# Kernel optimization log

Hardware: AMD Instinct MI355X
Metric: run time of the kernel (lower is better)

## Reference

```python
import jax, jax.numpy as jnp
import numpy as np

RADIUS = 0.5
NEG_INF = -jnp.inf


def setup_inputs() -> dict:
    key = jax.random.key(0)
    ks = jax.random.split(key, 10)
    N_q, N_o, pos_dim, latent_dim = 2048, 2048, 3, 64
    enc_dim = 3 * pos_dim  # q_pos, o_pos, rel
    inp = {
        "h_obs": jax.random.normal(ks[0], (N_o, latent_dim), dtype=jnp.float32),
        "x_obs": jax.random.normal(ks[1], (N_o, latent_dim), dtype=jnp.float32),
        "pos_obs": jax.random.uniform(ks[2], (N_o, pos_dim), dtype=jnp.float32),
        "pos_query": jax.random.uniform(ks[3], (N_q, pos_dim), dtype=jnp.float32),
        # kernel_mlp: Linear(enc_dim->latent) + ReLU + Linear(latent->1)
        "W1": jax.random.normal(ks[4], (enc_dim, latent_dim), dtype=jnp.float32) / np.sqrt(enc_dim),
        "b1": jnp.zeros((latent_dim,), dtype=jnp.float32),
        "W2": jax.random.normal(ks[5], (latent_dim, 1), dtype=jnp.float32) / np.sqrt(latent_dim),
        "b2": jnp.zeros((1,), dtype=jnp.float32),
        # value_proj: Linear(latent->latent)
        "Wv": jax.random.normal(ks[6], (latent_dim, latent_dim), dtype=jnp.float32) / np.sqrt(latent_dim),
        "bv": jnp.zeros((latent_dim,), dtype=jnp.float32),
    }
    return inp


def reference(h_obs, x_obs, pos_obs, pos_query, W1, b1, W2, b2, Wv, bv):
    # rel: [N_q, N_o, pos_dim]
    rel = pos_query[:, None, :] - pos_obs[None, :, :]
    N_q, N_o, _ = rel.shape
    pos_q_exp = jnp.broadcast_to(pos_query[:, None, :], rel.shape)
    pos_o_exp = jnp.broadcast_to(pos_obs[None, :, :], rel.shape)
    kernel_input = jnp.concatenate([pos_q_exp, pos_o_exp, rel], axis=-1)  # [N_q, N_o, 3*pos_dim]
    # small pointwise MLP over all pairs
    hidden = jax.nn.relu(jnp.einsum('qoe,el->qol', kernel_input, W1) + b1)  # [N_q, N_o, latent]
    logits = jnp.einsum('qol,lk->qok', hidden, W2)[..., 0] + b2[0]          # [N_q, N_o]
    # radius mask
    dist = jnp.linalg.norm(rel, axis=-1)
    logits = jnp.where(dist > RADIUS, NEG_INF, logits)
    # softmax over observations (dim=1)
    weights = jax.nn.softmax(logits, axis=1)  # [N_q, N_o]
    v = h_obs @ Wv + bv                        # [N_o, latent]
    h_query = weights @ v                      # [N_q, latent]
    return h_query
```

## Files before the change

kernel.cpp:

```cpp
#include <hip/hip_runtime.h>

#define NQ 2048
#define NO 2048
#define NOC 32

constexpr size_t OFF_T  = 0;
constexpr size_t OFF_PH = (size_t)NO * 64;
constexpr size_t OFF_PS = OFF_PH + (size_t)NOC * NQ * 64;

__global__ __launch_bounds__(256) void gano_prep(
    const float* __restrict__ pos_obs,
    const float* __restrict__ W1,
    float* __restrict__ T)
{
    int gid = blockIdx.x * 256 + threadIdx.x;
    int o = gid >> 6, l = gid & 63;
    float po0 = pos_obs[o * 3 + 0], po1 = pos_obs[o * 3 + 1], po2 = pos_obs[o * 3 + 2];
    float w3 = W1[3 * 64 + l], w4 = W1[4 * 64 + l], w5 = W1[5 * 64 + l];
    float w6 = W1[6 * 64 + l], w7 = W1[7 * 64 + l], w8 = W1[8 * 64 + l];
    T[(size_t)o * 64 + l] = po0 * (w3 - w6) + po1 * (w4 - w7) + po2 * (w5 - w8);
}

__global__ __launch_bounds__(256, 4) void gano_main(
    const float* __restrict__ T,
    const float* __restrict__ h_obs,
    const float* __restrict__ pos_obs,
    const float* __restrict__ pos_query,
    const float* __restrict__ W1,
    const float* __restrict__ b1,
    const float* __restrict__ W2,
    float* __restrict__ Ph,
    float* __restrict__ Ps)
{
    __shared__ float ue[64 * 64];
    __shared__ float sbuf[4 * 64];

    const int tid  = threadIdx.x;
    const int lane = tid & 63;
    const int wave = __builtin_amdgcn_readfirstlane(tid >> 6);
    const int qg = blockIdx.x >> 5;
    const int oc = blockIdx.x & 31;
    const int obase = oc * 64;
    const int q  = qg * 64 + lane;
    const int ow = wave * 16;

    float pq0 = pos_query[q * 3 + 0];
    float pq1 = pos_query[q * 3 + 1];
    float pq2 = pos_query[q * 3 + 2];

    float u[64];
#pragma unroll
    for (int l = 0; l < 64; ++l) {
        float a = b1[l];
        a += pq0 * W1[0 * 64 + l];
        a += pq1 * W1[1 * 64 + l];
        a += pq2 * W1[2 * 64 + l];
        a += pq0 * W1[6 * 64 + l];
        a += pq1 * W1[7 * 64 + l];
        a += pq2 * W1[8 * 64 + l];
        u[l] = a;
    }

    float spart = 0.f;
#pragma unroll 2
    for (int o = 0; o < 16; ++o) {
        const int toff = __builtin_amdgcn_readfirstlane((obase + ow + o) * 64);
        const float* __restrict__ trow = T + toff;
        float a0 = 0.f, a1 = 0.f, a2 = 0.f, a3 = 0.f;
#pragma unroll
        for (int l = 0; l < 64; l += 4) {
            a0 += W2[l + 0] * fmaxf(u[l + 0] + trow[l + 0], 0.f);
            a1 += W2[l + 1] * fmaxf(u[l + 1] + trow[l + 1], 0.f);
            a2 += W2[l + 2] * fmaxf(u[l + 2] + trow[l + 2], 0.f);
            a3 += W2[l + 3] * fmaxf(u[l + 3] + trow[l + 3], 0.f);
        }
        float lgo = (a0 + a1) + (a2 + a3);
        const int poff = __builtin_amdgcn_readfirstlane((obase + ow + o) * 3);
        float d0 = pq0 - pos_obs[poff + 0];
        float d1 = pq1 - pos_obs[poff + 1];
        float d2 = pq2 - pos_obs[poff + 2];
        float dd = d0 * d0 + d1 * d1 + d2 * d2;
        float ev = (dd > 0.25f) ? 0.f : __expf(lgo);
        spart += ev;
        ue[(ow + o) * 64 + lane] = ev;
    }
    sbuf[wave * 64 + lane] = spart;
    __syncthreads();

    float h0 = 0.f, h1 = 0.f, h2 = 0.f, h3 = 0.f, h4 = 0.f, h5 = 0.f, h6 = 0.f, h7 = 0.f;
    float h8 = 0.f, h9 = 0.f, hA = 0.f, hB = 0.f, hC = 0.f, hD = 0.f, hE = 0.f, hF = 0.f;
#pragma unroll 2
    for (int o = 0; o < 64; ++o) {
        float eo = ue[o * 64 + lane];
        const int hoff = __builtin_amdgcn_readfirstlane((obase + o) * 64 + ow);
        const float* __restrict__ hr = h_obs + hoff;
        h0 += eo * hr[0];  h1 += eo * hr[1];  h2 += eo * hr[2];  h3 += eo * hr[3];
        h4 += eo * hr[4];  h5 += eo * hr[5];  h6 += eo * hr[6];  h7 += eo * hr[7];
        h8 += eo * hr[8];  h9 += eo * hr[9];  hA += eo * hr[10]; hB += eo * hr[11];
        hC += eo * hr[12]; hD += eo * hr[13]; hE += eo * hr[14]; hF += eo * hr[15];
    }

    float* hp = Ph + ((size_t)oc * NQ + (size_t)qg * 64 + lane) * 64 + ow;
    ((float4*)hp)[0] = make_float4(h0, h1, h2, h3);
    ((float4*)hp)[1] = make_float4(h4, h5, h6, h7);
    ((float4*)hp)[2] = make_float4(h8, h9, hA, hB);
    ((float4*)hp)[3] = make_float4(hC, hD, hE, hF);
    if (wave == 0) {
        float s = sbuf[lane] + sbuf[64 + lane] + sbuf[128 + lane] + sbuf[192 + lane];
        Ps[(size_t)oc * NQ + (size_t)qg * 64 + lane] = s;
    }
}

__global__ __launch_bounds__(256, 2) void gano_comb(
    const float* __restrict__ Ph,
    const float* __restrict__ Ps,
    const float* __restrict__ Wv,
    const float* __restrict__ bv,
    float* __restrict__ out)
{
    __shared__ __align__(16) float wv[64 * 64];
    __shared__ __align__(16) float g[4 * 68];
    const int tid  = threadIdx.x;
    const int lane = tid & 63;
    const int wave = tid >> 6;
    const int q0 = blockIdx.x * 4;
    {
        const float4* src = (const float4*)Wv;
        float4* dst = (float4*)wv;
#pragma unroll
        for (int k = 0; k < 4; ++k) dst[tid + k * 256] = src[tid + k * 256];
    }
    {
        const int qi = wave, k = lane;
        float acc = 0.f;
#pragma unroll
        for (int c = 0; c < NOC; ++c)
            acc += Ph[((size_t)c * NQ + q0 + qi) * 64 + k];
        g[qi * 68 + k] = acc;
        if (k == 0) {
            float ss = 0.f;
#pragma unroll
            for (int c = 0; c < NOC; ++c) ss += Ps[(size_t)c * NQ + q0 + qi];
            g[qi * 68 + 64] = ss;
        }
    }
    __syncthreads();
    const float* gq = g + wave * 68;
    float inv = 1.0f / gq[64];
    float a0 = 0.f, a1 = 0.f, a2 = 0.f, a3 = 0.f;
#pragma unroll
    for (int kb = 0; kb < 16; ++kb) {
        float4 g4 = *(const float4*)(gq + kb * 4);
        a0 += g4.x * wv[(kb * 4 + 0) * 64 + lane];
        a1 += g4.y * wv[(kb * 4 + 1) * 64 + lane];
        a2 += g4.z * wv[(kb * 4 + 2) * 64 + lane];
        a3 += g4.w * wv[(kb * 4 + 3) * 64 + lane];
    }
    out[(size_t)(q0 + wave) * 64 + lane] = ((a0 + a1) + (a2 + a3)) * inv + bv[lane];
}

extern "C" void kernel_launch(void* const* d_in, const int* in_sizes, int n_in,
                              void* d_out, int out_size, void* d_ws, size_t ws_size,
                              hipStream_t stream) {
    const float* h_obs     = (const float*)d_in[0];
    const float* pos_obs   = (const float*)d_in[2];
    const float* pos_query = (const float*)d_in[3];
    const float* W1        = (const float*)d_in[4];
    const float* b1        = (const float*)d_in[5];
    const float* W2        = (const float*)d_in[6];
    const float* Wv        = (const float*)d_in[8];
    const float* bv        = (const float*)d_in[9];
    float* ws  = (float*)d_ws;
    float* out = (float*)d_out;

    gano_prep<<<dim3(NO * 64 / 256), dim3(256), 0, stream>>>(pos_obs, W1, ws + OFF_T);
    gano_main<<<dim3(1024), dim3(256), 0, stream>>>(ws + OFF_T, h_obs, pos_obs, pos_query,
                                                    W1, b1, W2, ws + OFF_PH, ws + OFF_PS);
    gano_comb<<<dim3(NQ / 4), dim3(256), 0, stream>>>(ws + OFF_PH, ws + OFF_PS, Wv, bv, out);
}
```

Before: 120.8 us.

## Transpose T table and stage per-query hidden bias in LDS to cut registers

New measurement: 117.7 us. -2.6%, faster.

```diff
diff --git a/kernel.cpp b/kernel.cpp
--- a/kernel.cpp
+++ b/kernel.cpp
@@ -4,25 +4,26 @@
 #define NO 2048
 #define NOC 32
 
-constexpr size_t OFF_T  = 0;
-constexpr size_t OFF_PH = (size_t)NO * 64;
+constexpr size_t OFF_TT = 0;
+constexpr size_t OFF_PH = (size_t)64 * NO;
 constexpr size_t OFF_PS = OFF_PH + (size_t)NOC * NQ * 64;
 
 __global__ __launch_bounds__(256) void gano_prep(
     const float* __restrict__ pos_obs,
     const float* __restrict__ W1,
-    float* __restrict__ T)
+    float* __restrict__ Tt)
 {
-    int gid = blockIdx.x * 256 + threadIdx.x;
-    int o = gid >> 6, l = gid & 63;
+    int idx = blockIdx.x * 256 + threadIdx.x;
+    int o = idx & (NO - 1);
+    int l = idx >> 11;
     float po0 = pos_obs[o * 3 + 0], po1 = pos_obs[o * 3 + 1], po2 = pos_obs[o * 3 + 2];
     float w3 = W1[3 * 64 + l], w4 = W1[4 * 64 + l], w5 = W1[5 * 64 + l];
     float w6 = W1[6 * 64 + l], w7 = W1[7 * 64 + l], w8 = W1[8 * 64 + l];
-    T[(size_t)o * 64 + l] = po0 * (w3 - w6) + po1 * (w4 - w7) + po2 * (w5 - w8);
+    Tt[(size_t)l * NO + o] = po0 * (w3 - w6) + po1 * (w4 - w7) + po2 * (w5 - w8);
 }
 
 __global__ __launch_bounds__(256, 4) void gano_main(
-    const float* __restrict__ T,
+    const float* __restrict__ Tt,
     const float* __restrict__ h_obs,
     const float* __restrict__ pos_obs,
     const float* __restrict__ pos_query,
@@ -32,6 +33,7 @@
     float* __restrict__ Ph,
     float* __restrict__ Ps)
 {
+    __shared__ __align__(16) float ut[16 * 64 * 4];
     __shared__ float ue[64 * 64];
     __shared__ float sbuf[4 * 64];
 
@@ -48,39 +50,52 @@
     float pq1 = pos_query[q * 3 + 1];
     float pq2 = pos_query[q * 3 + 2];
 
-    float u[64];
 #pragma unroll
-    for (int l = 0; l < 64; ++l) {
-        float a = b1[l];
-        a += pq0 * W1[0 * 64 + l];
-        a += pq1 * W1[1 * 64 + l];
-        a += pq2 * W1[2 * 64 + l];
-        a += pq0 * W1[6 * 64 + l];
-        a += pq1 * W1[7 * 64 + l];
-        a += pq2 * W1[8 * 64 + l];
-        u[l] = a;
+    for (int k = 0; k < 4; ++k) {
+        const int lb = wave * 4 + k;
+        float4 uv;
+        {
+            const int l = lb * 4;
+            uv.x = b1[l+0] + pq0*W1[l+0] + pq1*W1[64+l+0] + pq2*W1[128+l+0]
+                 + pq0*W1[384+l+0] + pq1*W1[448+l+0] + pq2*W1[512+l+0];
+            uv.y = b1[l+1] + pq0*W1[l+1] + pq1*W1[64+l+1] + pq2*W1[128+l+1]
+                 + pq0*W1[384+l+1] + pq1*W1[448+l+1] + pq2*W1[512+l+1];
+            uv.z = b1[l+2] + pq0*W1[l+2] + pq1*W1[64+l+2] + pq2*W1[128+l+2]
+                 + pq0*W1[384+l+2] + pq1*W1[448+l+2] + pq2*W1[512+l+2];
+            uv.w = b1[l+3] + pq0*W1[l+3] + pq1*W1[64+l+3] + pq2*W1[128+l+3]
+                 + pq0*W1[384+l+3] + pq1*W1[448+l+3] + pq2*W1[512+l+3];
+        }
+        *(float4*)(ut + (size_t)(lb * 64 + lane) * 4) = uv;
     }
+    __syncthreads();
 
+    float lg[16];
+#pragma unroll
+    for (int o = 0; o < 16; ++o) lg[o] = 0.f;
+#pragma unroll
+    for (int lb = 0; lb < 16; ++lb) {
+        float4 u4 = *(const float4*)(ut + (size_t)(lb * 64 + lane) * 4);
+#pragma unroll
+        for (int dl = 0; dl < 4; ++dl) {
+            const int l = lb * 4 + dl;
+            const int toff = __builtin_amdgcn_readfirstlane(l * NO + obase + ow);
+            const float* __restrict__ tr = Tt + toff;
+            const float ul = (dl == 0) ? u4.x : (dl == 1) ? u4.y : (dl == 2) ? u4.z : u4.w;
+            const float wl = W2[l];
+#pragma unroll
+            for (int o = 0; o < 16; ++o)
+                lg[o] += wl * fmaxf(ul + tr[o], 0.f);
+        }
+    }
     float spart = 0.f;
-#pragma unroll 2
+#pragma unroll
     for (int o = 0; o < 16; ++o) {
-        const int toff = __builtin_amdgcn_readfirstlane((obase + ow + o) * 64);
-        const float* __restrict__ trow = T + toff;
-        float a0 = 0.f, a1 = 0.f, a2 = 0.f, a3 = 0.f;
-#pragma unroll
-        for (int l = 0; l < 64; l += 4) {
-            a0 += W2[l + 0] * fmaxf(u[l + 0] + trow[l + 0], 0.f);
-            a1 += W2[l + 1] * fmaxf(u[l + 1] + trow[l + 1], 0.f);
-            a2 += W2[l + 2] * fmaxf(u[l + 2] + trow[l + 2], 0.f);
-            a3 += W2[l + 3] * fmaxf(u[l + 3] + trow[l + 3], 0.f);
-        }
-        float lgo = (a0 + a1) + (a2 + a3);
         const int poff = __builtin_amdgcn_readfirstlane((obase + ow + o) * 3);
         float d0 = pq0 - pos_obs[poff + 0];
         float d1 = pq1 - pos_obs[poff + 1];
         float d2 = pq2 - pos_obs[poff + 2];
         float dd = d0 * d0 + d1 * d1 + d2 * d2;
-        float ev = (dd > 0.25f) ? 0.f : __expf(lgo);
+        float ev = (dd > 0.25f) ? 0.f : __expf(lg[o]);
         spart += ev;
         ue[(ow + o) * 64 + lane] = ev;
     }
@@ -173,8 +188,8 @@
     float* ws  = (float*)d_ws;
     float* out = (float*)d_out;
 
-    gano_prep<<<dim3(NO * 64 / 256), dim3(256), 0, stream>>>(pos_obs, W1, ws + OFF_T);
-    gano_main<<<dim3(1024), dim3(256), 0, stream>>>(ws + OFF_T, h_obs, pos_obs, pos_query,
+    gano_prep<<<dim3(NO * 64 / 256), dim3(256), 0, stream>>>(pos_obs, W1, ws + OFF_TT);
+    gano_main<<<dim3(1024), dim3(256), 0, stream>>>(ws + OFF_TT, h_obs, pos_obs, pos_query,
                                                     W1, b1, W2, ws + OFF_PH, ws + OFF_PS);
     gano_comb<<<dim3(NQ / 4), dim3(256), 0, stream>>>(ws + OFF_PH, ws + OFF_PS, Wv, bv, out);
 }
```

## Fuse obs-projection prep into main kernel with LDS tables and smaller obs chunks

Applied to the files above, without the earlier changes.

After: 122.3 us. No clear change (+1.2%).

```diff
diff --git a/kernel.cpp b/kernel.cpp
--- a/kernel.cpp
+++ b/kernel.cpp
@@ -2,27 +2,12 @@
 
 #define NQ 2048
 #define NO 2048
-#define NOC 32
+#define NOC 64
 
-constexpr size_t OFF_T  = 0;
-constexpr size_t OFF_PH = (size_t)NO * 64;
-constexpr size_t OFF_PS = OFF_PH + (size_t)NOC * NQ * 64;
+constexpr size_t OFF_PH = 0;
+constexpr size_t OFF_PS = (size_t)NOC * NQ * 64;
 
-__global__ __launch_bounds__(256) void gano_prep(
-    const float* __restrict__ pos_obs,
-    const float* __restrict__ W1,
-    float* __restrict__ T)
-{
-    int gid = blockIdx.x * 256 + threadIdx.x;
-    int o = gid >> 6, l = gid & 63;
-    float po0 = pos_obs[o * 3 + 0], po1 = pos_obs[o * 3 + 1], po2 = pos_obs[o * 3 + 2];
-    float w3 = W1[3 * 64 + l], w4 = W1[4 * 64 + l], w5 = W1[5 * 64 + l];
-    float w6 = W1[6 * 64 + l], w7 = W1[7 * 64 + l], w8 = W1[8 * 64 + l];
-    T[(size_t)o * 64 + l] = po0 * (w3 - w6) + po1 * (w4 - w7) + po2 * (w5 - w8);
-}
-
-__global__ __launch_bounds__(256, 4) void gano_main(
-    const float* __restrict__ T,
+__global__ __launch_bounds__(256, 6) void gano_main(
     const float* __restrict__ h_obs,
     const float* __restrict__ pos_obs,
     const float* __restrict__ pos_query,
@@ -32,75 +17,100 @@
     float* __restrict__ Ph,
     float* __restrict__ Ps)
 {
-    __shared__ float ue[64 * 64];
+    __shared__ __align__(16) float wtab[64 * 8];
+    __shared__ __align__(16) float tl[64 * 32];
+    __shared__ float po[3 * 32];
+    __shared__ float ue[32 * 64];
     __shared__ float sbuf[4 * 64];
 
     const int tid  = threadIdx.x;
     const int lane = tid & 63;
     const int wave = __builtin_amdgcn_readfirstlane(tid >> 6);
-    const int qg = blockIdx.x >> 5;
-    const int oc = blockIdx.x & 31;
-    const int obase = oc * 64;
+    const int qg = blockIdx.x >> 6;
+    const int oc = blockIdx.x & 63;
+    const int obase = oc * 32;
     const int q  = qg * 64 + lane;
-    const int ow = wave * 16;
 
+    if (tid < 64) {
+        float w0 = W1[0*64+tid], w1_ = W1[1*64+tid], w2_ = W1[2*64+tid];
+        float w3 = W1[3*64+tid], w4  = W1[4*64+tid], w5  = W1[5*64+tid];
+        float w6 = W1[6*64+tid], w7  = W1[7*64+tid], w8  = W1[8*64+tid];
+        float* r = wtab + tid * 8;
+        r[0] = w0 + w6;  r[1] = w1_ + w7;  r[2] = w2_ + w8;
+        r[3] = b1[tid];  r[4] = W2[tid];
+        r[5] = w3 - w6;  r[6] = w4 - w7;   r[7] = w5 - w8;
+    }
+    if (tid < 32) {
+        po[tid]      = pos_obs[(obase + tid) * 3 + 0];
+        po[32 + tid] = pos_obs[(obase + tid) * 3 + 1];
+        po[64 + tid] = pos_obs[(obase + tid) * 3 + 2];
+    }
     float pq0 = pos_query[q * 3 + 0];
     float pq1 = pos_query[q * 3 + 1];
     float pq2 = pos_query[q * 3 + 2];
+    __syncthreads();
 
-    float u[64];
+    {
+        const int o = lane & 31, half = lane >> 5;
+        float p0 = po[o], p1 = po[32 + o], p2 = po[64 + o];
 #pragma unroll
+        for (int j = 0; j < 8; ++j) {
+            int l = wave * 16 + j * 2 + half;
+            const float* r = wtab + l * 8;
+            tl[l * 32 + o] = p0 * r[5] + p1 * r[6] + p2 * r[7];
+        }
+    }
+    __syncthreads();
+
+    float lg[8];
+#pragma unroll
+    for (int o = 0; o < 8; ++o) lg[o] = 0.f;
+    const int ow = wave * 8;
+#pragma unroll 16
     for (int l = 0; l < 64; ++l) {
-        float a = b1[l];
-        a += pq0 * W1[0 * 64 + l];
-        a += pq1 * W1[1 * 64 + l];
-        a += pq2 * W1[2 * 64 + l];
-        a += pq0 * W1[6 * 64 + l];
-        a += pq1 * W1[7 * 64 + l];
-        a += pq2 * W1[8 * 64 + l];
-        u[l] = a;
+        float4 c4 = *(const float4*)(wtab + l * 8);
+        float wl  = wtab[l * 8 + 4];
+        float u   = fmaf(pq2, c4.z, fmaf(pq1, c4.y, fmaf(pq0, c4.x, c4.w)));
+        float4 ta = *(const float4*)(tl + l * 32 + ow);
+        float4 tb = *(const float4*)(tl + l * 32 + ow + 4);
+        lg[0] += wl * fmaxf(u + ta.x, 0.f);
+        lg[1] += wl * fmaxf(u + ta.y, 0.f);
+        lg[2] += wl * fmaxf(u + ta.z, 0.f);
+        lg[3] += wl * fmaxf(u + ta.w, 0.f);
+        lg[4] += wl * fmaxf(u + tb.x, 0.f);
+        lg[5] += wl * fmaxf(u + tb.y, 0.f);
+        lg[6] += wl * fmaxf(u + tb.z, 0.f);
+        lg[7] += wl * fmaxf(u + tb.w, 0.f);
     }
-
     float spart = 0.f;
-#pragma unroll 2
-    for (int o = 0; o < 16; ++o) {
-        const int toff = __builtin_amdgcn_readfirstlane((obase + ow + o) * 64);
-        const float* __restrict__ trow = T + toff;
-        float a0 = 0.f, a1 = 0.f, a2 = 0.f, a3 = 0.f;
 #pragma unroll
-        for (int l = 0; l < 64; l += 4) {
-            a0 += W2[l + 0] * fmaxf(u[l + 0] + trow[l + 0], 0.f);
-            a1 += W2[l + 1] * fmaxf(u[l + 1] + trow[l + 1], 0.f);
-            a2 += W2[l + 2] * fmaxf(u[l + 2] + trow[l + 2], 0.f);
-            a3 += W2[l + 3] * fmaxf(u[l + 3] + trow[l + 3], 0.f);
-        }
-        float lgo = (a0 + a1) + (a2 + a3);
-        const int poff = __builtin_amdgcn_readfirstlane((obase + ow + o) * 3);
-        float d0 = pq0 - pos_obs[poff + 0];
-        float d1 = pq1 - pos_obs[poff + 1];
-        float d2 = pq2 - pos_obs[poff + 2];
+    for (int o = 0; o < 8; ++o) {
+        float d0 = pq0 - po[ow + o];
+        float d1 = pq1 - po[32 + ow + o];
+        float d2 = pq2 - po[64 + ow + o];
         float dd = d0 * d0 + d1 * d1 + d2 * d2;
-        float ev = (dd > 0.25f) ? 0.f : __expf(lgo);
+        float ev = (dd > 0.25f) ? 0.f : __expf(lg[o]);
         spart += ev;
         ue[(ow + o) * 64 + lane] = ev;
     }
     sbuf[wave * 64 + lane] = spart;
     __syncthreads();
 
+    const int lw = wave * 16;
     float h0 = 0.f, h1 = 0.f, h2 = 0.f, h3 = 0.f, h4 = 0.f, h5 = 0.f, h6 = 0.f, h7 = 0.f;
     float h8 = 0.f, h9 = 0.f, hA = 0.f, hB = 0.f, hC = 0.f, hD = 0.f, hE = 0.f, hF = 0.f;
-#pragma unroll 2
-    for (int o = 0; o < 64; ++o) {
+#pragma unroll 4
+    for (int o = 0; o < 32; ++o) {
         float eo = ue[o * 64 + lane];
-        const int hoff = __builtin_amdgcn_readfirstlane((obase + o) * 64 + ow);
-        const float* __restrict__ hr = h_obs + hoff;
-        h0 += eo * hr[0];  h1 += eo * hr[1];  h2 += eo * hr[2];  h3 += eo * hr[3];
-        h4 += eo * hr[4];  h5 += eo * hr[5];  h6 += eo * hr[6];  h7 += eo * hr[7];
-        h8 += eo * hr[8];  h9 += eo * hr[9];  hA += eo * hr[10]; hB += eo * hr[11];
-        hC += eo * hr[12]; hD += eo * hr[13]; hE += eo * hr[14]; hF += eo * hr[15];
+        const float4* hr = (const float4*)(h_obs + (size_t)(obase + o) * 64 + lw);
+        float4 v0 = hr[0], v1 = hr[1], v2 = hr[2], v3 = hr[3];
+        h0 += eo * v0.x; h1 += eo * v0.y; h2 += eo * v0.z; h3 += eo * v0.w;
+        h4 += eo * v1.x; h5 += eo * v1.y; h6 += eo * v1.z; h7 += eo * v1.w;
+        h8 += eo * v2.x; h9 += eo * v2.y; hA += eo * v2.z; hB += eo * v2.w;
+        hC += eo * v3.x; hD += eo * v3.y; hE += eo * v3.z; hF += eo * v3.w;
     }
 
-    float* hp = Ph + ((size_t)oc * NQ + (size_t)qg * 64 + lane) * 64 + ow;
+    float* hp = Ph + ((size_t)oc * NQ + (size_t)qg * 64 + lane) * 64 + lw;
     ((float4*)hp)[0] = make_float4(h0, h1, h2, h3);
     ((float4*)hp)[1] = make_float4(h4, h5, h6, h7);
     ((float4*)hp)[2] = make_float4(h8, h9, hA, hB);
@@ -133,13 +143,13 @@
     {
         const int qi = wave, k = lane;
         float acc = 0.f;
-#pragma unroll
+#pragma unroll 8
         for (int c = 0; c < NOC; ++c)
             acc += Ph[((size_t)c * NQ + q0 + qi) * 64 + k];
         g[qi * 68 + k] = acc;
         if (k == 0) {
             float ss = 0.f;
-#pragma unroll
+#pragma unroll 8
             for (int c = 0; c < NOC; ++c) ss += Ps[(size_t)c * NQ + q0 + qi];
             g[qi * 68 + 64] = ss;
         }
@@ -173,8 +183,7 @@
     float* ws  = (float*)d_ws;
     float* out = (float*)d_out;
 
-    gano_prep<<<dim3(NO * 64 / 256), dim3(256), 0, stream>>>(pos_obs, W1, ws + OFF_T);
-    gano_main<<<dim3(1024), dim3(256), 0, stream>>>(ws + OFF_T, h_obs, pos_obs, pos_query,
+    gano_main<<<dim3(2048), dim3(256), 0, stream>>>(h_obs, pos_obs, pos_query,
                                                     W1, b1, W2, ws + OFF_PH, ws + OFF_PS);
     gano_comb<<<dim3(NQ / 4), dim3(256), 0, stream>>>(ws + OFF_PH, ws + OFF_PS, Wv, bv, out);
 }
```
